# Optimization experiments

Measured on AMD Instinct MI355X. Metric: run time of the kernel, lower is better.

Reference implementation:

```python
import jax, jax.numpy as jnp
import numpy as np

B, C, N = 16, 256, 4096

def setup_inputs() -> dict:
    key = jax.random.key(0)
    k1, k2 = jax.random.split(key)
    x = jax.random.normal(k1, (B, C, 3, N), dtype=jnp.float32)
    # torch nn.Linear weight [out_features, in_features], scaled like kaiming-uniform-ish
    W = jax.random.normal(k2, (C, C), dtype=jnp.float32) * (1.0 / np.sqrt(C))
    return {"x": x, "W": W}

def reference(x, W):
    # d[b,c,k,n] = sum_i W[c,i] * x[b,i,k,n]  (Linear over channel dim, no bias)
    d = jnp.einsum('ci,bikn->bckn', W, x)
    # dot product over the 3-vector axis -> [B, C, N]
    dotprod = jnp.sum(x * d, axis=2)
    # argmax over samples -> [B, C]
    idx = jnp.argmax(dotprod, axis=-1)
    # gather the 3-vector at the max index: x_max[b,c,k] = x[b,c,k,idx[b,c]]
    x_max = jnp.take_along_axis(x, idx[:, :, None, None], axis=3)[..., 0]
    return x_max  # [B, C, 3]
```

## Files before the change

kernel.cpp:

```cpp
#include <hip/hip_runtime.h>

typedef _Float16 half8 __attribute__((ext_vector_type(8)));
typedef _Float16 half4 __attribute__((ext_vector_type(4)));
typedef float    f32x4 __attribute__((ext_vector_type(4)));
typedef unsigned long long u64;

#define B_ 16
#define C_ 256
#define N_ 4096
#define TAU 0.02f

#define SWZ16(k, n, i) (((((k) * 32 + (n)) * 256) + (i)) ^ ((((n) >> 1) & 7) << 3))

__device__ __forceinline__ u64 shfl_xor_u64(u64 v, int m) {
    unsigned lo = __shfl_xor((unsigned)v, m);
    unsigned hi = __shfl_xor((unsigned)(v >> 32), m);
    return ((u64)hi << 32) | lo;
}
__device__ __forceinline__ void t2m(u64& A1, u64& A2, u64 B1, u64 B2) {
    bool aw = A1 > B1;
    u64 T1 = aw ? A1 : B1;
    u64 lv = aw ? B1 : A1;
    u64 wv = aw ? A2 : B2;
    A2 = lv > wv ? lv : wv;
    A1 = T1;
}
__device__ __forceinline__ float unkey(unsigned key) {
    unsigned u = (key & 0x80000000u) ? (key ^ 0x80000000u) : ~key;
    return __uint_as_float(u);
}

__global__ void prep_w(const float* __restrict__ W,
                       _Float16* __restrict__ WfH, _Float16* __restrict__ WfL) {
    int t = blockIdx.x * 256 + threadIdx.x;
    int l = t & 63, g = t >> 6;
    int s = g & 7, cb = g >> 3;
    int c = cb * 16 + (l & 15);
    int i0 = s * 32 + (l >> 4) * 8;
    int base = ((cb * 8 + s) * 64 + l) * 8;
#pragma unroll
    for (int j = 0; j < 8; ++j) {
        float w = 16.0f * W[c * C_ + i0 + j];
        _Float16 h  = (_Float16)w;
        _Float16 lo = (_Float16)(w - (float)h);
        WfH[base + j] = h;
        WfL[base + j] = lo;
    }
}

__global__ __launch_bounds__(512, 4) void vn_main(
    const float* __restrict__ x,
    const _Float16* __restrict__ WfH, const _Float16* __restrict__ WfL,
    ulonglong2* __restrict__ btop)
{
    __shared__ __align__(16) _Float16 X[3 * 32 * 256];

    const int tid  = threadIdx.x;
    const int lane = tid & 63;
    const int wid  = tid >> 6;
    const int b    = blockIdx.x >> 7;
    const int nb   = blockIdx.x & 127;
    const int n0   = nb << 5;
    const int g    = lane >> 4;
    const int t16  = lane & 15;

    const float* xb = x + ((size_t)(b * 768) << 12);

    const int npair = tid & 15;
    const int rg    = tid >> 4;
    float2 vb[2][4];

#define LOADP(P, PR)                                                              \
    do { int rgp = (P) * 32 + rg; int i4 = rgp / 3, kk = rgp - 3 * i4;            \
        _Pragma("unroll") for (int rr = 0; rr < 4; ++rr)                          \
            vb[PR][rr] = *(const float2*)(xb +                                    \
                (((i4 * 4 + rr) * 3 + kk) << 12) + n0 + 2 * npair);               \
    } while (0)

#define WRITEP(P, PR)                                                             \
    do { int rgp = (P) * 32 + rg; int i4 = rgp / 3, kk = rgp - 3 * i4;            \
        _Pragma("unroll") for (int nn = 0; nn < 2; ++nn) {                        \
            int n = 2 * npair + nn;                                               \
            half4 h;                                                              \
            h[0] = (_Float16)(nn ? vb[PR][0].y : vb[PR][0].x);                    \
            h[1] = (_Float16)(nn ? vb[PR][1].y : vb[PR][1].x);                    \
            h[2] = (_Float16)(nn ? vb[PR][2].y : vb[PR][2].x);                    \
            h[3] = (_Float16)(nn ? vb[PR][3].y : vb[PR][3].x);                    \
            *(half4*)(&X[SWZ16(kk, n, i4 * 4)]) = h;                              \
        } } while (0)

    LOADP(0, 0);
#pragma unroll
    for (int p = 0; p < 6; ++p) {
        if (p < 5) LOADP(p + 1, (p + 1) & 1);
        WRITEP(p, p & 1);
    }
    __syncthreads();

    f32x4 acc[3][2][2];
    const f32x4 zero = {0.f, 0.f, 0.f, 0.f};
#pragma unroll
    for (int k = 0; k < 3; ++k)
#pragma unroll
        for (int cf = 0; cf < 2; ++cf)
#pragma unroll
            for (int nf = 0; nf < 2; ++nf) acc[k][cf][nf] = zero;

    half8 ah[2][2], al[2];

#define WOFF(CF, S) ((((((wid << 1) + (CF)) << 3) + (S)) * 64 + lane) << 3)

#pragma unroll
    for (int cf = 0; cf < 2; ++cf) {
        ah[0][cf] = *(const half8*)(WfH + WOFF(cf, 0));
        al[cf]    = *(const half8*)(WfL + WOFF(cf, 0));
    }

#pragma unroll
    for (int s = 0; s < 8; ++s) {
        const int P = s & 1;
        half8 bh[3][2];
#pragma unroll
        for (int k = 0; k < 3; ++k)
#pragma unroll
            for (int nf = 0; nf < 2; ++nf)
                bh[k][nf] = *(const half8*)(&X[SWZ16(k, (nf << 4) | t16, (s << 5) + (g << 3))]);
        if (s < 7)
#pragma unroll
            for (int cf = 0; cf < 2; ++cf)
                ah[P ^ 1][cf] = *(const half8*)(WfH + WOFF(cf, s + 1));
#pragma unroll
        for (int k = 0; k < 3; ++k)
#pragma unroll
            for (int cf = 0; cf < 2; ++cf)
#pragma unroll
                for (int nf = 0; nf < 2; ++nf)
                    acc[k][cf][nf] = __builtin_amdgcn_mfma_f32_16x16x32_f16(ah[P][cf], bh[k][nf], acc[k][cf][nf], 0, 0, 0);
#pragma unroll
        for (int k = 0; k < 3; ++k)
#pragma unroll
            for (int cf = 0; cf < 2; ++cf)
#pragma unroll
                for (int nf = 0; nf < 2; ++nf)
                    acc[k][cf][nf] = __builtin_amdgcn_mfma_f32_16x16x32_f16(al[cf], bh[k][nf], acc[k][cf][nf], 0, 0, 0);
        if (s < 7)
#pragma unroll
            for (int cf = 0; cf < 2; ++cf)
                al[cf] = *(const half8*)(WfL + WOFF(cf, s + 1));
    }

#pragma unroll
    for (int cf = 0; cf < 2; ++cf) {
        half4 xrA[3], xrB[3];
        const int ci = (wid << 5) + (cf << 4) + (g << 2);
#pragma unroll
        for (int k = 0; k < 3; ++k) {
            xrA[k] = *(const half4*)(&X[SWZ16(k, t16,      ci)]);
            xrB[k] = *(const half4*)(&X[SWZ16(k, 16 | t16, ci)]);
        }
#pragma unroll
        for (int r = 0; r < 4; ++r) {
            float dpA = 0.f, dpB = 0.f;
#pragma unroll
            for (int k = 0; k < 3; ++k) {
                dpA += (float)xrA[k][r] * acc[k][cf][0][r];
                dpB += (float)xrB[k][r] * acc[k][cf][1][r];
            }
            dpA *= 0.0625f; dpB *= 0.0625f;
            unsigned uA = __float_as_uint(dpA);
            unsigned keyA = (uA & 0x80000000u) ? ~uA : (uA | 0x80000000u);
            unsigned uB = __float_as_uint(dpB);
            unsigned keyB = (uB & 0x80000000u) ? ~uB : (uB | 0x80000000u);
            int nA = n0 + t16, nB = n0 + 16 + t16;
            u64 A1 = ((u64)keyA << 32) | (unsigned)(~nA);
            u64 A2 = 0;
            u64 B1 = ((u64)keyB << 32) | (unsigned)(~nB);
            t2m(A1, A2, B1, 0);
#pragma unroll
            for (int m = 1; m <= 8; m <<= 1) {
                u64 C1 = shfl_xor_u64(A1, m);
                u64 C2 = shfl_xor_u64(A2, m);
                t2m(A1, A2, C1, C2);
            }
            if (t16 == 0) {
                int c = ci + r;
                btop[(size_t)((b << 8) + c) * 128 + nb] = make_ulonglong2(A1, A2);
            }
        }
    }
}

__global__ void phase2(const float* __restrict__ x, const float* __restrict__ W,
                       const ulonglong2* __restrict__ btop, float* __restrict__ out)
{
    const int bc = blockIdx.x;
    const int b = bc >> 8, c = bc & 255;
    const int lane = threadIdx.x;

    u64 A1 = 0, A2 = 0;
    u64 e1[2];
#pragma unroll
    for (int t = 0; t < 2; ++t) {
        ulonglong2 e = btop[(size_t)bc * 128 + t * 64 + lane];
        e1[t] = e.x;
        t2m(A1, A2, e.x, e.y);
    }
#pragma unroll
    for (int m = 1; m <= 32; m <<= 1) {
        u64 B1 = shfl_xor_u64(A1, m);
        u64 B2 = shfl_xor_u64(A2, m);
        t2m(A1, A2, B1, B2);
    }
    float v1 = unkey((unsigned)(A1 >> 32));
    float v2 = unkey((unsigned)(A2 >> 32));
    int winner = (int)(~(unsigned)A1) & (N_ - 1);

    if (!(v1 - v2 > TAU)) {
        float bv = -3.4e38f; int bi = 0x7fffffff;
#pragma unroll
        for (int t = 0; t < 2; ++t) {
            bool flag = unkey((unsigned)(e1[t] >> 32)) >= v1 - TAU;
            unsigned long long mask = __ballot(flag);
            while (mask) {
                int src = __builtin_ctzll(mask);
                mask &= mask - 1;
                int win = t * 64 + src;
                for (int ch = 0; ch < 4; ++ch) {
                    int nbase = win * 32 + ch * 8;
                    float accv[8];
#pragma unroll
                    for (int m2 = 0; m2 < 8; ++m2) accv[m2] = 0.f;
                    float xc[3][8];
#pragma unroll
                    for (int k = 0; k < 3; ++k) {
                        const float* p = x + (((size_t)bc * 3 + k) << 12) + nbase;
#pragma unroll
                        for (int m2 = 0; m2 < 8; ++m2) xc[k][m2] = p[m2];
                    }
                    for (int q = 0; q < 4; ++q) {
                        int i = lane + (q << 6);
                        float wq = W[c * C_ + i];
#pragma unroll
                        for (int k = 0; k < 3; ++k) {
                            const float* p = x + ((((size_t)b * C_ + i) * 3 + k) << 12) + nbase;
#pragma unroll
                            for (int m2 = 0; m2 < 8; ++m2)
                                accv[m2] += wq * p[m2] * xc[k][m2];
                        }
                    }
#pragma unroll
                    for (int m2 = 0; m2 < 8; ++m2) {
#pragma unroll
                        for (int mm = 1; mm <= 32; mm <<= 1)
                            accv[m2] += __shfl_xor(accv[m2], mm);
                        int n = nbase + m2;
                        if (accv[m2] > bv || (accv[m2] == bv && n < bi)) { bv = accv[m2]; bi = n; }
                    }
                }
            }
        }
        winner = bi;
    }

    if (lane < 3)
        out[bc * 3 + lane] = x[(((size_t)bc * 3 + lane) << 12) + winner];
}

extern "C" void kernel_launch(void* const* d_in, const int* in_sizes, int n_in,
                              void* d_out, int out_size, void* d_ws, size_t ws_size,
                              hipStream_t stream) {
    const float* x = (const float*)d_in[0];
    const float* W = (const float*)d_in[1];
    float* out = (float*)d_out;

    _Float16*   WfH  = (_Float16*)d_ws;
    _Float16*   WfL  = (_Float16*)((char*)d_ws + 131072);
    ulonglong2* btop = (ulonglong2*)((char*)d_ws + 262144);

    prep_w<<<32, 256, 0, stream>>>(W, WfH, WfL);
    vn_main<<<B_ * 128, 512, 0, stream>>>(x, WfH, WfL, btop);
    phase2<<<B_ * C_, 64, 0, stream>>>(x, W, btop, out);
}
```

Baseline: 118.4 us.

## Restructure main kernel into 128-sample tiles with double-buffered per-k staging

The main kernel now uses 1024-thread blocks that each cover 128 samples instead of 32, giving 512 blocks instead of 2048. It processes the three vector components one after another and double-buffers the shared-memory tile, so the global loads for the next component overlap the MFMAs on the current one. Each wave now owns 16 output channels, which cuts the duplicated weight fetches and per-block staging overhead. The cost is larger blocks with 128 KB of shared memory each, lower occupancy, and extra barriers between components. The output layout of partial top-2 results is unchanged, so the second-phase kernel still works.

```diff
diff --git a/kernel.cpp b/kernel.cpp
--- a/kernel.cpp
+++ b/kernel.cpp
@@ -10,7 +10,7 @@
 #define N_ 4096
 #define TAU 0.02f
 
-#define SWZ16(k, n, i) (((((k) * 32 + (n)) * 256) + (i)) ^ ((((n) >> 1) & 7) << 3))
+#define XI(n, i) ( ((n) << 8) | (((((i) >> 3) ^ ((n) & 7)) & 31) << 3) | ((i) & 7) )
 
 __device__ __forceinline__ u64 shfl_xor_u64(u64 v, int m) {
     unsigned lo = __shfl_xor((unsigned)v, m);
@@ -48,133 +48,110 @@
     }
 }
 
-__global__ __launch_bounds__(512, 4) void vn_main(
+__global__ __launch_bounds__(1024) void vn_main(
     const float* __restrict__ x,
     const _Float16* __restrict__ WfH, const _Float16* __restrict__ WfL,
     ulonglong2* __restrict__ btop)
 {
-    __shared__ __align__(16) _Float16 X[3 * 32 * 256];
+    __shared__ __align__(16) _Float16 X[2][128 * 256];
 
     const int tid  = threadIdx.x;
     const int lane = tid & 63;
     const int wid  = tid >> 6;
-    const int b    = blockIdx.x >> 7;
-    const int nb   = blockIdx.x & 127;
-    const int n0   = nb << 5;
+    const int b    = blockIdx.x >> 5;
+    const int nb   = blockIdx.x & 31;
+    const int n0   = nb << 7;
     const int g    = lane >> 4;
     const int t16  = lane & 15;
 
     const float* xb = x + ((size_t)(b * 768) << 12);
 
-    const int npair = tid & 15;
-    const int rg    = tid >> 4;
-    float2 vb[2][4];
-
-#define LOADP(P, PR)                                                              \
-    do { int rgp = (P) * 32 + rg; int i4 = rgp / 3, kk = rgp - 3 * i4;            \
-        _Pragma("unroll") for (int rr = 0; rr < 4; ++rr)                          \
-            vb[PR][rr] = *(const float2*)(xb +                                    \
-                (((i4 * 4 + rr) * 3 + kk) << 12) + n0 + 2 * npair);               \
+    const int nl = tid & 31;
+    const int qb = tid >> 5;
+
+    f32x4 vs[4];
+
+#define SLOAD(T, K)  do { int i0_ = ((qb) + (T) * 32) << 2;                        \
+    _Pragma("unroll") for (int r = 0; r < 4; ++r)                                  \
+        vs[r] = *(const f32x4*)(xb + (((i0_ + r) * 3 + (K)) << 12) + n0 + (nl << 2)); \
     } while (0)
 
-#define WRITEP(P, PR)                                                             \
-    do { int rgp = (P) * 32 + rg; int i4 = rgp / 3, kk = rgp - 3 * i4;            \
-        _Pragma("unroll") for (int nn = 0; nn < 2; ++nn) {                        \
-            int n = 2 * npair + nn;                                               \
-            half4 h;                                                              \
-            h[0] = (_Float16)(nn ? vb[PR][0].y : vb[PR][0].x);                    \
-            h[1] = (_Float16)(nn ? vb[PR][1].y : vb[PR][1].x);                    \
-            h[2] = (_Float16)(nn ? vb[PR][2].y : vb[PR][2].x);                    \
-            h[3] = (_Float16)(nn ? vb[PR][3].y : vb[PR][3].x);                    \
-            *(half4*)(&X[SWZ16(kk, n, i4 * 4)]) = h;                              \
-        } } while (0)
-
-    LOADP(0, 0);
-#pragma unroll
-    for (int p = 0; p < 6; ++p) {
-        if (p < 5) LOADP(p + 1, (p + 1) & 1);
-        WRITEP(p, p & 1);
-    }
+#define SWRITE(T, BUF) do { int i0_ = ((qb) + (T) * 32) << 2; int n4_ = nl << 2;   \
+    _Pragma("unroll") for (int j = 0; j < 4; ++j) {                                \
+        half4 h; h[0] = (_Float16)vs[0][j]; h[1] = (_Float16)vs[1][j];             \
+        h[2] = (_Float16)vs[2][j]; h[3] = (_Float16)vs[3][j];                      \
+        *(half4*)(&X[BUF][XI(n4_ + j, i0_)]) = h; }                                \
+    } while (0)
+
+#define WOFF(S) ((((wid << 3) + (S)) * 64 + lane) << 3)
+
+    half8 ah[2], al;
+
+    ah[0] = *(const half8*)(WfH + WOFF(0));
+    al    = *(const half8*)(WfL + WOFF(0));
+    SLOAD(0, 0); SWRITE(0, 0);
+    SLOAD(1, 0); SWRITE(1, 0);
     __syncthreads();
 
-    f32x4 acc[3][2][2];
-    const f32x4 zero = {0.f, 0.f, 0.f, 0.f};
-#pragma unroll
-    for (int k = 0; k < 3; ++k)
-#pragma unroll
-        for (int cf = 0; cf < 2; ++cf)
-#pragma unroll
-            for (int nf = 0; nf < 2; ++nf) acc[k][cf][nf] = zero;
-
-    half8 ah[2][2], al[2];
-
-#define WOFF(CF, S) ((((((wid << 1) + (CF)) << 3) + (S)) * 64 + lane) << 3)
-
-#pragma unroll
-    for (int cf = 0; cf < 2; ++cf) {
-        ah[0][cf] = *(const half8*)(WfH + WOFF(cf, 0));
-        al[cf]    = *(const half8*)(WfL + WOFF(cf, 0));
-    }
-
-#pragma unroll
-    for (int s = 0; s < 8; ++s) {
-        const int P = s & 1;
-        half8 bh[3][2];
-#pragma unroll
-        for (int k = 0; k < 3; ++k)
-#pragma unroll
-            for (int nf = 0; nf < 2; ++nf)
-                bh[k][nf] = *(const half8*)(&X[SWZ16(k, (nf << 4) | t16, (s << 5) + (g << 3))]);
-        if (s < 7)
-#pragma unroll
-            for (int cf = 0; cf < 2; ++cf)
-                ah[P ^ 1][cf] = *(const half8*)(WfH + WOFF(cf, s + 1));
-#pragma unroll
-        for (int k = 0; k < 3; ++k)
-#pragma unroll
-            for (int cf = 0; cf < 2; ++cf)
-#pragma unroll
-                for (int nf = 0; nf < 2; ++nf)
-                    acc[k][cf][nf] = __builtin_amdgcn_mfma_f32_16x16x32_f16(ah[P][cf], bh[k][nf], acc[k][cf][nf], 0, 0, 0);
-#pragma unroll
-        for (int k = 0; k < 3; ++k)
-#pragma unroll
-            for (int cf = 0; cf < 2; ++cf)
-#pragma unroll
-                for (int nf = 0; nf < 2; ++nf)
-                    acc[k][cf][nf] = __builtin_amdgcn_mfma_f32_16x16x32_f16(al[cf], bh[k][nf], acc[k][cf][nf], 0, 0, 0);
-        if (s < 7)
-#pragma unroll
-            for (int cf = 0; cf < 2; ++cf)
-                al[cf] = *(const half8*)(WfL + WOFF(cf, s + 1));
-    }
-
-#pragma unroll
-    for (int cf = 0; cf < 2; ++cf) {
-        half4 xrA[3], xrB[3];
-        const int ci = (wid << 5) + (cf << 4) + (g << 2);
-#pragma unroll
-        for (int k = 0; k < 3; ++k) {
-            xrA[k] = *(const half4*)(&X[SWZ16(k, t16,      ci)]);
-            xrB[k] = *(const half4*)(&X[SWZ16(k, 16 | t16, ci)]);
-        }
-#pragma unroll
-        for (int r = 0; r < 4; ++r) {
-            float dpA = 0.f, dpB = 0.f;
-#pragma unroll
-            for (int k = 0; k < 3; ++k) {
-                dpA += (float)xrA[k][r] * acc[k][cf][0][r];
-                dpB += (float)xrB[k][r] * acc[k][cf][1][r];
-            }
-            dpA *= 0.0625f; dpB *= 0.0625f;
-            unsigned uA = __float_as_uint(dpA);
-            unsigned keyA = (uA & 0x80000000u) ? ~uA : (uA | 0x80000000u);
-            unsigned uB = __float_as_uint(dpB);
-            unsigned keyB = (uB & 0x80000000u) ? ~uB : (uB | 0x80000000u);
-            int nA = n0 + t16, nB = n0 + 16 + t16;
-            u64 A1 = ((u64)keyA << 32) | (unsigned)(~nA);
+    f32x4 dp[8];
+#pragma unroll
+    for (int nf = 0; nf < 8; ++nf) dp[nf] = (f32x4){0.f, 0.f, 0.f, 0.f};
+
+#pragma unroll
+    for (int k = 0; k < 3; ++k) {
+        const int bk = k & 1;
+        f32x4 acc[8];
+#pragma unroll
+        for (int nf = 0; nf < 8; ++nf) acc[nf] = (f32x4){0.f, 0.f, 0.f, 0.f};
+
+        if (k < 2) SLOAD(0, k + 1);
+
+#pragma unroll
+        for (int s = 0; s < 8; ++s) {
+            const int P = s & 1;
+            if (s < 7) ah[P ^ 1] = *(const half8*)(WfH + WOFF(s + 1));
+#pragma unroll
+            for (int nf = 0; nf < 8; ++nf) {
+                const half8 bh = *(const half8*)(&X[bk][XI(t16 + (nf << 4), (s << 5) + (g << 3))]);
+                acc[nf] = __builtin_amdgcn_mfma_f32_16x16x32_f16(ah[P], bh, acc[nf], 0, 0, 0);
+                acc[nf] = __builtin_amdgcn_mfma_f32_16x16x32_f16(al,    bh, acc[nf], 0, 0, 0);
+            }
+            if (s < 7) al = *(const half8*)(WfL + WOFF(s + 1));
+            if (s == 3 && k < 2) { SWRITE(0, bk ^ 1); SLOAD(1, k + 1); }
+        }
+
+#pragma unroll
+        for (int nf = 0; nf < 8; ++nf) {
+            const half4 xr = *(const half4*)(&X[bk][XI(t16 + (nf << 4), (wid << 4) + (g << 2))]);
+#pragma unroll
+            for (int r = 0; r < 4; ++r)
+                dp[nf][r] += (float)xr[r] * acc[nf][r];
+        }
+
+        if (k < 2) {
+            SWRITE(1, bk ^ 1);
+            ah[0] = *(const half8*)(WfH + WOFF(0));
+            al    = *(const half8*)(WfL + WOFF(0));
+        }
+        __syncthreads();
+    }
+
+    const int cr = (wid << 4) + (g << 2);
+#pragma unroll
+    for (int r = 0; r < 4; ++r) {
+#pragma unroll
+        for (int w = 0; w < 4; ++w) {
+            float d0 = dp[2 * w][r]     * 0.0625f;
+            float d1 = dp[2 * w + 1][r] * 0.0625f;
+            unsigned u0 = __float_as_uint(d0);
+            unsigned k0 = (u0 & 0x80000000u) ? ~u0 : (u0 | 0x80000000u);
+            unsigned u1 = __float_as_uint(d1);
+            unsigned k1 = (u1 & 0x80000000u) ? ~u1 : (u1 | 0x80000000u);
+            int nA = n0 + (w << 5) + t16;
+            int nB = nA + 16;
+            u64 A1 = ((u64)k0 << 32) | (unsigned)(~nA);
             u64 A2 = 0;
-            u64 B1 = ((u64)keyB << 32) | (unsigned)(~nB);
+            u64 B1 = ((u64)k1 << 32) | (unsigned)(~nB);
             t2m(A1, A2, B1, 0);
 #pragma unroll
             for (int m = 1; m <= 8; m <<= 1) {
@@ -183,8 +160,8 @@
                 t2m(A1, A2, C1, C2);
             }
             if (t16 == 0) {
-                int c = ci + r;
-                btop[(size_t)((b << 8) + c) * 128 + nb] = make_ulonglong2(A1, A2);
+                int c = cr + r;
+                btop[(size_t)((b << 8) + c) * 128 + (nb << 2) + w] = make_ulonglong2(A1, A2);
             }
         }
     }
@@ -278,6 +255,6 @@
     ulonglong2* btop = (ulonglong2*)((char*)d_ws + 262144);
 
     prep_w<<<32, 256, 0, stream>>>(W, WfH, WfL);
-    vn_main<<<B_ * 128, 512, 0, stream>>>(x, WfH, WfL, btop);
+    vn_main<<<B_ * 32, 1024, 0, stream>>>(x, WfH, WfL, btop);
     phase2<<<B_ * C_, 64, 0, stream>>>(x, W, btop, out);
 }
```

After: 194.4 us. +64.1%, slower.
